# Kernel tuning notes

Hardware: AMD Instinct MI355X
Metric: run time of the kernel (lower is better)

Reference implementation:

```python
import jax, jax.numpy as jnp
import numpy as np

B, N, D, H = 2, 2048, 2048, 16
HD = D // H  # head_dim = 128


def _rope(x, cos, sin):
    # x: [B,H,N,HD]; cos/sin: [N,HD]. use_real=True, use_real_unbind_dim=-1 (interleaved pairs).
    xr = x[..., 0::2]
    xi = x[..., 1::2]
    x_rot = jnp.stack([-xi, xr], axis=-1).reshape(x.shape)
    return x * cos[None, None] + x_rot * sin[None, None]


def setup_inputs() -> dict:
    key = jax.random.key(0)
    ks = jax.random.split(key, 10)
    x = jax.random.normal(ks[0], (B, N, D), dtype=jnp.float32)
    # realistic RoPE tables
    inv_freq = 1.0 / (10000.0 ** (np.arange(0, HD, 2, dtype=np.float32) / HD))
    t = np.arange(N, dtype=np.float32)
    ang = np.einsum('n,f->nf', t, inv_freq)           # [N, HD/2]
    ang = np.repeat(ang, 2, axis=-1)                  # [N, HD] interleaved
    cos = jnp.asarray(np.cos(ang))
    sin = jnp.asarray(np.sin(ang))
    s = 0.02
    Wq = jax.random.normal(ks[1], (D, D), dtype=jnp.float32) * s
    Wk = jax.random.normal(ks[2], (D, D), dtype=jnp.float32) * s
    Wv = jax.random.normal(ks[3], (D, D), dtype=jnp.float32) * s
    Wo = jax.random.normal(ks[4], (D, D), dtype=jnp.float32) * s
    bq = jnp.zeros((D,), jnp.float32)
    bk = jnp.zeros((D,), jnp.float32)
    bv = jnp.zeros((D,), jnp.float32)
    bo = jnp.zeros((D,), jnp.float32)
    return {"x": x, "cos": cos, "sin": sin, "Wq": Wq, "bq": bq, "Wk": Wk,
            "bk": bk, "Wv": Wv, "bv": bv, "Wo": Wo, "bo": bo}


def reference(x, cos, sin, Wq, bq, Wk, bk, Wv, bv, Wo, bo):
    scale = HD ** -0.5
    q = x @ Wq + bq
    k = x @ Wk + bk
    v = x @ Wv + bv
    # b n (h c) -> b h n c
    def split_heads(t):
        return t.reshape(B, N, H, HD).transpose(0, 2, 1, 3)
    q, k, v = split_heads(q), split_heads(k), split_heads(v)
    q = q * scale  # module's dp_scale
    q = _rope(q, cos, sin)
    k = _rope(k, cos, sin)
    # flash_attn_func(softmax_scale=None) applies head_dim^-0.5 AGAIN -> effective HD^-1
    logits = jnp.einsum('bhqc,bhkc->bhqk', q, k) * scale
    attn = jax.nn.softmax(logits, axis=-1)
    o = jnp.einsum('bhqk,bhkc->bhqc', attn, v)
    o = o.transpose(0, 2, 1, 3).reshape(B, N, D)  # b h n c -> b n (h c)
    return o @ Wo + bo
```

## Files before the change

kernel.cpp:

```cpp
#include <hip/hip_runtime.h>

typedef unsigned short u16;
typedef __attribute__((ext_vector_type(8))) short bfx8;
typedef __attribute__((ext_vector_type(4))) float fx4;
typedef __attribute__((ext_vector_type(4))) unsigned short u16x4;

#define MFMA_BF16(a,b,c) __builtin_amdgcn_mfma_f32_16x16x32_bf16((a),(b),(c),0,0,0)

#define BATCH 2
#define SEQ   2048
#define DM    2048
#define NH    16
#define HD    128
#define MR    4096

__device__ __forceinline__ u16 f2bf(float f){
  union{float f; unsigned u;} v; v.f = f;
  unsigned r = v.u + 0x7FFFu + ((v.u >> 16) & 1u);
  return (u16)(r >> 16);
}
__device__ __forceinline__ unsigned cvtpk(float lo, float hi){
  unsigned r;
  asm("v_cvt_pk_bf16_f32 %0, %1, %2" : "=v"(r) : "v"(lo), "v"(hi));
  return r;
}
__device__ __forceinline__ void gll16(const void* g, void* l){
  __builtin_amdgcn_global_load_lds(
      (const __attribute__((address_space(1))) void*)g,
      (__attribute__((address_space(3))) void*)l, 16, 0, 0);
}

__global__ __launch_bounds__(256) void k_cast(const float* __restrict__ in,
                                              u16* __restrict__ o, int n4){
  int gid = blockIdx.x*256 + threadIdx.x;
  if (gid >= n4) return;
  float4 x = ((const float4*)in)[gid];
  u16x4 v = {f2bf(x.x), f2bf(x.y), f2bf(x.z), f2bf(x.w)};
  ((u16x4*)o)[gid] = v;
}

__global__ __launch_bounds__(256) void k_twcat(const float* __restrict__ Wq,
                                               const float* __restrict__ Wk,
                                               const float* __restrict__ Wv,
                                               u16* __restrict__ Th){
  __shared__ float T[64][65];
  int z = blockIdx.z;
  const float* W = (z==0) ? Wq : (z==1) ? Wk : Wv;
  int n0 = blockIdx.x*64, k0 = blockIdx.y*64;
  int t = threadIdx.x;
  int r = t>>2, c = (t&3)*16;
  const float* src = W + (size_t)(k0+r)*DM + n0 + c;
  #pragma unroll
  for (int j=0;j<4;j++){
    float4 v = *(const float4*)(src + 4*j);
    T[r][c+4*j+0]=v.x; T[r][c+4*j+1]=v.y; T[r][c+4*j+2]=v.z; T[r][c+4*j+3]=v.w;
  }
  __syncthreads();
  int nr = t>>2, kc = (t&3)*16;
  size_t ob = (size_t)(z*DM + n0+nr)*DM + k0 + kc;
  #pragma unroll
  for (int j=0;j<16;j+=4){
    u16x4 vh;
    #pragma unroll
    for (int q=0;q<4;q++) vh[q] = f2bf(T[kc+j+q][nr]);
    *(u16x4*)(Th+ob+j)=vh;
  }
}

__global__ __launch_bounds__(256) void k_tw(const float* __restrict__ W, u16* __restrict__ Th){
  __shared__ float T[64][65];
  int n0 = blockIdx.x*64, k0 = blockIdx.y*64;
  int t = threadIdx.x;
  int r = t>>2, c = (t&3)*16;
  const float* src = W + (size_t)(k0+r)*DM + n0 + c;
  #pragma unroll
  for (int j=0;j<4;j++){
    float4 v = *(const float4*)(src + 4*j);
    T[r][c+4*j+0]=v.x; T[r][c+4*j+1]=v.y; T[r][c+4*j+2]=v.z; T[r][c+4*j+3]=v.w;
  }
  __syncthreads();
  int nr = t>>2, kc = (t&3)*16;
  size_t ob = (size_t)(n0+nr)*DM + k0 + kc;
  #pragma unroll
  for (int j=0;j<16;j+=4){
    u16x4 vh;
    #pragma unroll
    for (int q=0;q<4;q++) vh[q] = f2bf(T[kc+j+q][nr]);
    *(u16x4*)(Th+ob+j)=vh;
  }
}

__global__ __launch_bounds__(256) void k_gemm_qkv(
    const u16* __restrict__ A, const u16* __restrict__ B,
    const float* __restrict__ bqp, const float* __restrict__ bkp, const float* __restrict__ bvp,
    const float* __restrict__ cs, const float* __restrict__ sn,
    u16* __restrict__ qb, u16* __restrict__ kb, u16* __restrict__ vt)
{
  __shared__ u16 sA[128*64], sB[128*64];
  const int K = DM;
  const int tid = threadIdx.x;
  const int lane = tid & 63;
  const int w = tid >> 6;
  const int g = lane >> 4, qi = lane & 15;
  const int wr = w >> 1, wc = w & 1;
  const int bm = blockIdx.y * 128;
  const int bn = blockIdx.x * 128;

  int r_[4], sc_[4];
  #pragma unroll
  for (int i=0;i<4;i++){
    int off = w*4096 + i*1024 + lane*16;
    int r = off>>7, cb = off&127;
    r_[i] = r; sc_[i] = (cb ^ ((r&7)<<4)) >> 1;
  }

  fx4 acc[4][4] = {};

  for (int k0 = 0; k0 < K; k0 += 64){
    __syncthreads();
    #pragma unroll
    for (int i=0;i<4;i++){
      gll16(A + (size_t)(bm + r_[i])*K + k0 + sc_[i], &sA[w*2048 + i*512]);
      gll16(B + (size_t)(bn + r_[i])*K + k0 + sc_[i], &sB[w*2048 + i*512]);
    }
    __syncthreads();

    #pragma unroll
    for (int kk=0;kk<2;kk++){
      const int cb = kk*64 + g*16;
      bfx8 fa[4], fb[4];
      #pragma unroll
      for (int m=0;m<4;m++){
        int row = wr*64 + m*16 + qi;
        fa[m] = *(const bfx8*)((const char*)sA + row*128 + (cb ^ ((row&7)<<4)));
      }
      #pragma unroll
      for (int n=0;n<4;n++){
        int row = wc*64 + n*16 + qi;
        fb[n] = *(const bfx8*)((const char*)sB + row*128 + (cb ^ ((row&7)<<4)));
      }
      #pragma unroll
      for (int m=0;m<4;m++)
        #pragma unroll
        for (int n=0;n<4;n++)
          acc[m][n] = MFMA_BF16(fa[m], fb[n], acc[m][n]);
    }
  }

  const int sec = bn >> 11;
  if (sec < 2){
    u16* dst = sec ? kb : qb;
    const float* bias = sec ? bkp : bqp;
    const float qs = sec ? 1.0f : (1.4426950408889634f/128.0f);
    #pragma unroll
    for (int m=0;m<4;m++){
      #pragma unroll
      for (int n=0;n<4;n++){
        int col = bn + wc*64 + n*16 + qi;
        int cq = col & 2047, hh = cq>>7, d = cq&127;
        float bc = bias[cq];
        float sgn = (d&1) ? 1.0f : -1.0f;
        #pragma unroll
        for (int r=0;r<4;r++){
          int row = bm + wr*64 + m*16 + g*4 + r;
          int bI = row>>11, nr2 = row&2047;
          float v = (acc[m][n][r] + bc)*qs;
          float p = __shfl_xor(v, 1, 64);
          float c = cs[nr2*HD + d], s = sn[nr2*HD + d];
          float y = v*c + sgn*p*s;
          dst[((size_t)(bI*NH+hh)*SEQ + nr2)*HD + d] = f2bf(y);
        }
      }
    }
  } else {
    #pragma unroll
    for (int m=0;m<4;m++){
      #pragma unroll
      for (int n=0;n<4;n++){
        int col = bn + wc*64 + n*16 + qi;
        int cv = col & 2047, hh = cv>>7, d = cv&127;
        float bc = bvp[cv];
        int row0 = bm + wr*64 + m*16 + g*4;
        int bI = row0>>11, n0_ = row0&2047;
        u16x4 pk;
        #pragma unroll
        for (int r=0;r<4;r++) pk[r] = f2bf(acc[m][n][r] + bc);
        *(u16x4*)(vt + ((size_t)(bI*NH+hh)*HD + d)*SEQ + n0_) = pk;
      }
    }
  }
}

__global__ __launch_bounds__(256) void k_gemm(
    const u16* __restrict__ A, const u16* __restrict__ B,
    const float* __restrict__ bias, float* __restrict__ C,
    int M, int N, int K)
{
  __shared__ u16 sA[128*64], sB[128*64];
  const int tid = threadIdx.x;
  const int lane = tid & 63;
  const int w = tid >> 6;
  const int g = lane >> 4, qi = lane & 15;
  const int wr = w >> 1, wc = w & 1;
  const int bm = blockIdx.y * 128;
  const int bn = blockIdx.x * 128;

  int r_[4], sc_[4];
  #pragma unroll
  for (int i=0;i<4;i++){
    int off = w*4096 + i*1024 + lane*16;
    int r = off>>7, cb = off&127;
    r_[i] = r; sc_[i] = (cb ^ ((r&7)<<4)) >> 1;
  }

  fx4 acc[4][4] = {};

  for (int k0 = 0; k0 < K; k0 += 64){
    __syncthreads();
    #pragma unroll
    for (int i=0;i<4;i++){
      gll16(A + (size_t)(bm + r_[i])*K + k0 + sc_[i], &sA[w*2048 + i*512]);
      gll16(B + (size_t)(bn + r_[i])*K + k0 + sc_[i], &sB[w*2048 + i*512]);
    }
    __syncthreads();

    #pragma unroll
    for (int kk=0;kk<2;kk++){
      const int cb = kk*64 + g*16;
      bfx8 fa[4], fb[4];
      #pragma unroll
      for (int m=0;m<4;m++){
        int row = wr*64 + m*16 + qi;
        fa[m] = *(const bfx8*)((const char*)sA + row*128 + (cb ^ ((row&7)<<4)));
      }
      #pragma unroll
      for (int n=0;n<4;n++){
        int row = wc*64 + n*16 + qi;
        fb[n] = *(const bfx8*)((const char*)sB + row*128 + (cb ^ ((row&7)<<4)));
      }
      #pragma unroll
      for (int m=0;m<4;m++)
        #pragma unroll
        for (int n=0;n<4;n++)
          acc[m][n] = MFMA_BF16(fa[m], fb[n], acc[m][n]);
    }
  }

  #pragma unroll
  for (int m=0;m<4;m++){
    #pragma unroll
    for (int n=0;n<4;n++){
      int col = bn + wc*64 + n*16 + qi;
      float bc = bias[col];
      #pragma unroll
      for (int r=0;r<4;r++){
        int row = bm + wr*64 + m*16 + g*4 + r;
        C[(size_t)row*N + col] = acc[m][n][r] + bc;
      }
    }
  }
}

__global__ __launch_bounds__(256) void k_flash(const u16* __restrict__ Q, const u16* __restrict__ Kb,
                                               const u16* __restrict__ Vt, u16* __restrict__ O){
  __shared__ union SM {
    struct { u16 k[2][64*128]; u16 v[2][128*64]; } s;
    u16 ob[128*128];
  } sm;
  const int tid = threadIdx.x, lane = tid & 63, w = tid >> 6;
  const int bid = blockIdx.x;
  const int qt = bid & 15, h = (bid>>4)&15, b = bid>>8;
  const int bh = b*NH + h;
  const int qb0 = qt*128;
  const int g = lane >> 4, qi = lane & 15;

  bfx8 qf[2][4];
  #pragma unroll
  for (int j=0;j<2;j++){
    const u16* qp = Q + ((size_t)bh*SEQ + qb0 + w*32 + j*16 + qi)*HD + g*8;
    #pragma unroll
    for (int ks=0; ks<4; ++ks) qf[j][ks] = *(const bfx8*)(qp + ks*32);
  }

  size_t kbase[4], vbase[4];
  #pragma unroll
  for (int i=0;i<4;i++){
    int off = w*4096 + i*1024 + lane*16;
    int kr = off>>8, kc = off&255;
    int kcs = kc ^ ((kr&7)<<4);
    kbase[i] = ((size_t)bh*SEQ + kr)*HD + (kcs>>1);
    int vr = off>>7, vc = off&127;
    int vcs = vc ^ ((vr&7)<<4);
    vbase[i] = ((size_t)bh*HD + vr)*SEQ + (vcs>>1);
  }

#define STG(bf_, kv_, i_) \
    gll16(Kb + kbase[i_] + (size_t)(kv_)*HD, &sm.s.k[bf_][w*2048 + i_*512]); \
    gll16(Vt + vbase[i_] + (kv_),            &sm.s.v[bf_][w*2048 + i_*512]);
#define STAGE(bf_, kv_) do { STG(bf_,kv_,0) STG(bf_,kv_,1) STG(bf_,kv_,2) STG(bf_,kv_,3) } while(0)

  fx4 accO[2][8] = {};
  float mrun[2] = {-1e30f,-1e30f}, lrun[2] = {0.f,0.f};

  STAGE(0, 0);
  int buf = 0;

  for (int t=0; t<32; ++t){
    if (t < 31){
      STAGE(buf^1, (t+1)*64);
      asm volatile("s_waitcnt vmcnt(8)" ::: "memory");
    } else {
      asm volatile("s_waitcnt vmcnt(0)" ::: "memory");
    }
    __builtin_amdgcn_s_barrier();
    const u16* sk = sm.s.k[buf];
    const u16* sv = sm.s.v[buf];

    fx4 st[2][4] = {};
    __builtin_amdgcn_s_setprio(1);
    #pragma unroll
    for (int ks=0; ks<4; ++ks){
      bfx8 kf[4];
      #pragma unroll
      for (int n=0;n<4;n++){
        int row = n*16 + qi;
        int cb = ks*64 + g*16;
        kf[n] = *(const bfx8*)((const char*)sk + row*256 + (cb ^ ((row&7)<<4)));
      }
      #pragma unroll
      for (int n=0;n<4;n++){
        st[0][n] = MFMA_BF16(kf[n], qf[0][ks], st[0][n]);
        st[1][n] = MFMA_BF16(kf[n], qf[1][ks], st[1][n]);
      }
    }
    __builtin_amdgcn_s_setprio(0);

    float pmv[2];
    #pragma unroll
    for (int j=0;j<2;j++){
      float pm = st[j][0][0];
      #pragma unroll
      for (int n=0;n<4;n++)
        #pragma unroll
        for (int r=0;r<4;r++) pm = fmaxf(pm, st[j][n][r]);
      pm = fmaxf(pm, __shfl_xor(pm, 16, 64));
      pm = fmaxf(pm, __shfl_xor(pm, 32, 64));
      pmv[j] = pm;
    }
    if (!__all((pmv[0] <= mrun[0] + 11.0f) && (pmv[1] <= mrun[1] + 11.0f))){
      #pragma unroll
      for (int j=0;j<2;j++){
        float mn = fmaxf(mrun[j], pmv[j]);
        float al = exp2f(mrun[j] - mn);
        lrun[j] *= al;
        #pragma unroll
        for (int nn=0;nn<8;nn++) accO[j][nn] = accO[j][nn]*al;
        mrun[j] = mn;
      }
    }
    #pragma unroll
    for (int j=0;j<2;j++){
      float ps = 0.f;
      #pragma unroll
      for (int n=0;n<4;n++)
        #pragma unroll
        for (int r=0;r<4;r++){
          float p = exp2f(st[j][n][r] - mrun[j]);
          st[j][n][r] = p;
          ps += p;
        }
      ps += __shfl_xor(ps, 16, 64);
      ps += __shfl_xor(ps, 32, 64);
      lrun[j] += ps;
    }

    int pkl[2][4], pkh[2][4];
    #pragma unroll
    for (int j=0;j<2;j++)
      #pragma unroll
      for (int n=0;n<4;n++){
        pkl[j][n] = (int)cvtpk(st[j][n][0], st[j][n][1]);
        pkh[j][n] = (int)cvtpk(st[j][n][2], st[j][n][3]);
      }

    const int s0 = qi + 16*((2*g)&3);
    const int s1 = qi + 16*((2*g+1)&3);
    const bool hi = (g>>1) != 0;

    #pragma unroll
    for (int ks=0; ks<2; ++ks){
      bfx8 pv[2];
      #pragma unroll
      for (int j=0;j<2;j++){
        int cl0 = pkl[j][2*ks],   ch0 = pkh[j][2*ks];
        int cl1 = pkl[j][2*ks+1], ch1 = pkh[j][2*ks+1];
        int t00 = __shfl(cl0, s0, 64), t10 = __shfl(cl1, s0, 64);
        int t01 = __shfl(ch0, s0, 64), t11 = __shfl(ch1, s0, 64);
        int t02 = __shfl(cl0, s1, 64), t12 = __shfl(cl1, s1, 64);
        int t03 = __shfl(ch0, s1, 64), t13 = __shfl(ch1, s1, 64);
        union { bfx8 v; int u[4]; } pu;
        pu.u[0] = hi ? t10 : t00;
        pu.u[1] = hi ? t11 : t01;
        pu.u[2] = hi ? t12 : t02;
        pu.u[3] = hi ? t13 : t03;
        pv[j] = pu.v;
      }
      __builtin_amdgcn_s_setprio(1);
      #pragma unroll
      for (int nn=0;nn<8;nn++){
        int row = nn*16 + qi;
        int cb = ks*64 + g*16;
        bfx8 vf = *(const bfx8*)((const char*)sv + row*128 + (cb ^ ((row&7)<<4)));
        accO[0][nn] = MFMA_BF16(vf, pv[0], accO[0][nn]);
        accO[1][nn] = MFMA_BF16(vf, pv[1], accO[1][nn]);
      }
      __builtin_amdgcn_s_setprio(0);
    }
    __builtin_amdgcn_s_barrier();
    buf ^= 1;
  }
#undef STAGE
#undef STG

  #pragma unroll
  for (int j=0;j<2;j++){
    float inv = 1.0f / lrun[j];
    int q = w*32 + j*16 + qi;
    #pragma unroll
    for (int nn=0;nn<8;nn++)
      #pragma unroll
      for (int r=0;r<4;r++){
        int d = nn*16 + g*4 + r;
        *(u16*)((char*)sm.ob + q*256 + ((d*2) ^ ((q&7)<<4))) = f2bf(accO[j][nn][r]*inv);
      }
  }
  __syncthreads();
  {
    int q2 = tid>>1, c0 = (tid&1)*64;
    u16* dst = O + (size_t)(b*SEQ + qb0 + q2)*DM + h*HD + c0;
    #pragma unroll
    for (int jj=0;jj<8;jj++){
      int d0 = c0 + jj*8;
      bfx8 v = *(const bfx8*)((const char*)sm.ob + q2*256 + ((d0*2) ^ ((q2&7)<<4)));
      *(bfx8*)(dst + jj*8) = v;
    }
  }
}

extern "C" void kernel_launch(void* const* d_in, const int* in_sizes, int n_in,
                              void* d_out, int out_size, void* d_ws, size_t ws_size,
                              hipStream_t stream){
  (void)in_sizes; (void)n_in; (void)out_size; (void)ws_size;
  const float* x  = (const float*)d_in[0];
  const float* cs = (const float*)d_in[1];
  const float* sn = (const float*)d_in[2];
  const float* Wq = (const float*)d_in[3];
  const float* bq = (const float*)d_in[4];
  const float* Wk = (const float*)d_in[5];
  const float* bk = (const float*)d_in[6];
  const float* Wv = (const float*)d_in[7];
  const float* bv = (const float*)d_in[8];
  const float* Wo = (const float*)d_in[9];
  const float* bo = (const float*)d_in[10];
  float* out = (float*)d_out;

  char* ws = (char*)d_ws;
  const size_t MB = 1048576;
  u16* xb   = (u16*)(ws);
  u16* wt   = (u16*)(ws + 16*MB);
  u16* qb   = (u16*)(ws + 40*MB);
  u16* kb   = (u16*)(ws + 56*MB);
  u16* vt   = (u16*)(ws + 72*MB);
  u16* ob16 = (u16*)(ws + 88*MB);

  k_cast<<<8192,256,0,stream>>>(x, xb, 2097152);
  k_twcat<<<dim3(32,32,3),256,0,stream>>>(Wq, Wk, Wv, wt);
  k_gemm_qkv<<<dim3(48,32),256,0,stream>>>(xb, wt, bq, bk, bv, cs, sn, qb, kb, vt);

  k_flash<<<512,256,0,stream>>>(qb, kb, vt, ob16);

  k_tw<<<dim3(32,32),256,0,stream>>>(Wo, wt);
  k_gemm<<<dim3(16,32),256,0,stream>>>(ob16, wt, bo, out, MR, DM, DM);
}
```

Before: 355.8 us.

## Halve flash-attention tile to 64 query rows with single-buffered split K/V staging

The attention kernel now uses 2 waves and 64 query rows per block, with twice as many blocks. The double-buffered K/V shared memory becomes a single buffer. K for the next step is loaded right after the QK product, and V right after the PV product, with waits and barriers placed between the phases. Cross-lane max and sum shuffles are moved off the common path: the max is reduced only when a rescale is needed, and the row sum only once at the end. The smaller shared-memory footprint aims to raise occupancy, but it doubles how often K/V are loaded per query and shortens the window for hiding load latency.

```diff
diff --git a/kernel.cpp b/kernel.cpp
--- a/kernel.cpp
+++ b/kernel.cpp
@@ -261,17 +261,17 @@
   }
 }
 
-__global__ __launch_bounds__(256) void k_flash(const u16* __restrict__ Q, const u16* __restrict__ Kb,
+__global__ __launch_bounds__(128) void k_flash(const u16* __restrict__ Q, const u16* __restrict__ Kb,
                                                const u16* __restrict__ Vt, u16* __restrict__ O){
   __shared__ union SM {
-    struct { u16 k[2][64*128]; u16 v[2][128*64]; } s;
-    u16 ob[128*128];
+    struct { u16 k[64*128]; u16 v[128*64]; } s;
+    u16 ob[64*128];
   } sm;
   const int tid = threadIdx.x, lane = tid & 63, w = tid >> 6;
   const int bid = blockIdx.x;
-  const int qt = bid & 15, h = (bid>>4)&15, b = bid>>8;
+  const int qt = bid & 31, h = (bid>>5)&15, b = bid>>9;
   const int bh = b*NH + h;
-  const int qb0 = qt*128;
+  const int qb0 = qt*64;
   const int g = lane >> 4, qi = lane & 15;
 
   bfx8 qf[2][4];
@@ -282,10 +282,10 @@
     for (int ks=0; ks<4; ++ks) qf[j][ks] = *(const bfx8*)(qp + ks*32);
   }
 
-  size_t kbase[4], vbase[4];
-  #pragma unroll
-  for (int i=0;i<4;i++){
-    int off = w*4096 + i*1024 + lane*16;
+  size_t kbase[8], vbase[8];
+  #pragma unroll
+  for (int i=0;i<8;i++){
+    int off = w*8192 + i*1024 + lane*16;
     int kr = off>>8, kc = off&255;
     int kcs = kc ^ ((kr&7)<<4);
     kbase[i] = ((size_t)bh*SEQ + kr)*HD + (kcs>>1);
@@ -294,27 +294,21 @@
     vbase[i] = ((size_t)bh*HD + vr)*SEQ + (vcs>>1);
   }
 
-#define STG(bf_, kv_, i_) \
-    gll16(Kb + kbase[i_] + (size_t)(kv_)*HD, &sm.s.k[bf_][w*2048 + i_*512]); \
-    gll16(Vt + vbase[i_] + (kv_),            &sm.s.v[bf_][w*2048 + i_*512]);
-#define STAGE(bf_, kv_) do { STG(bf_,kv_,0) STG(bf_,kv_,1) STG(bf_,kv_,2) STG(bf_,kv_,3) } while(0)
+#define STAGE_K(kv_) do { _Pragma("unroll") \
+    for (int i_=0;i_<8;i_++) gll16(Kb + kbase[i_] + (size_t)(kv_)*HD, &sm.s.k[w*4096 + i_*512]); } while(0)
+#define STAGE_V(kv_) do { _Pragma("unroll") \
+    for (int i_=0;i_<8;i_++) gll16(Vt + vbase[i_] + (kv_),            &sm.s.v[w*4096 + i_*512]); } while(0)
 
   fx4 accO[2][8] = {};
-  float mrun[2] = {-1e30f,-1e30f}, lrun[2] = {0.f,0.f};
-
-  STAGE(0, 0);
-  int buf = 0;
+  float mrun[2] = {-1e30f,-1e30f};
+  float lrun[2] = {0.f,0.f};
+
+  STAGE_K(0);
+  STAGE_V(0);
 
   for (int t=0; t<32; ++t){
-    if (t < 31){
-      STAGE(buf^1, (t+1)*64);
-      asm volatile("s_waitcnt vmcnt(8)" ::: "memory");
-    } else {
-      asm volatile("s_waitcnt vmcnt(0)" ::: "memory");
-    }
+    asm volatile("s_waitcnt vmcnt(8)" ::: "memory");
     __builtin_amdgcn_s_barrier();
-    const u16* sk = sm.s.k[buf];
-    const u16* sv = sm.s.v[buf];
 
     fx4 st[2][4] = {};
     __builtin_amdgcn_s_setprio(1);
@@ -325,7 +319,7 @@
       for (int n=0;n<4;n++){
         int row = n*16 + qi;
         int cb = ks*64 + g*16;
-        kf[n] = *(const bfx8*)((const char*)sk + row*256 + (cb ^ ((row&7)<<4)));
+        kf[n] = *(const bfx8*)((const char*)sm.s.k + row*256 + (cb ^ ((row&7)<<4)));
       }
       #pragma unroll
       for (int n=0;n<4;n++){
@@ -334,6 +328,8 @@
       }
     }
     __builtin_amdgcn_s_setprio(0);
+    __builtin_amdgcn_s_barrier();
+    if (t < 31) STAGE_K(t*64 + 64);
 
     float pmv[2];
     #pragma unroll
@@ -343,14 +339,15 @@
       for (int n=0;n<4;n++)
         #pragma unroll
         for (int r=0;r<4;r++) pm = fmaxf(pm, st[j][n][r]);
-      pm = fmaxf(pm, __shfl_xor(pm, 16, 64));
-      pm = fmaxf(pm, __shfl_xor(pm, 32, 64));
       pmv[j] = pm;
     }
     if (!__all((pmv[0] <= mrun[0] + 11.0f) && (pmv[1] <= mrun[1] + 11.0f))){
       #pragma unroll
       for (int j=0;j<2;j++){
-        float mn = fmaxf(mrun[j], pmv[j]);
+        float pq = pmv[j];
+        pq = fmaxf(pq, __shfl_xor(pq, 16, 64));
+        pq = fmaxf(pq, __shfl_xor(pq, 32, 64));
+        float mn = fmaxf(mrun[j], pq);
         float al = exp2f(mrun[j] - mn);
         lrun[j] *= al;
         #pragma unroll
@@ -369,8 +366,6 @@
           st[j][n][r] = p;
           ps += p;
         }
-      ps += __shfl_xor(ps, 16, 64);
-      ps += __shfl_xor(ps, 32, 64);
       lrun[j] += ps;
     }
 
@@ -382,6 +377,10 @@
         pkl[j][n] = (int)cvtpk(st[j][n][0], st[j][n][1]);
         pkh[j][n] = (int)cvtpk(st[j][n][2], st[j][n][3]);
       }
+
+    if (t < 31) asm volatile("s_waitcnt vmcnt(8)" ::: "memory");
+    else        asm volatile("s_waitcnt vmcnt(0)" ::: "memory");
+    __builtin_amdgcn_s_barrier();
 
     const int s0 = qi + 16*((2*g)&3);
     const int s1 = qi + 16*((2*g+1)&3);
@@ -410,21 +409,24 @@
       for (int nn=0;nn<8;nn++){
         int row = nn*16 + qi;
         int cb = ks*64 + g*16;
-        bfx8 vf = *(const bfx8*)((const char*)sv + row*128 + (cb ^ ((row&7)<<4)));
+        bfx8 vf = *(const bfx8*)((const char*)sm.s.v + row*128 + (cb ^ ((row&7)<<4)));
         accO[0][nn] = MFMA_BF16(vf, pv[0], accO[0][nn]);
         accO[1][nn] = MFMA_BF16(vf, pv[1], accO[1][nn]);
       }
       __builtin_amdgcn_s_setprio(0);
     }
     __builtin_amdgcn_s_barrier();
-    buf ^= 1;
-  }
-#undef STAGE
-#undef STG
+    if (t < 31) STAGE_V(t*64 + 64);
+  }
+#undef STAGE_K
+#undef STAGE_V
 
   #pragma unroll
   for (int j=0;j<2;j++){
-    float inv = 1.0f / lrun[j];
+    float l = lrun[j];
+    l += __shfl_xor(l, 16, 64);
+    l += __shfl_xor(l, 32, 64);
+    float inv = 1.0f / l;
     int q = w*32 + j*16 + qi;
     #pragma unroll
     for (int nn=0;nn<8;nn++)
@@ -477,7 +479,7 @@
   k_twcat<<<dim3(32,32,3),256,0,stream>>>(Wq, Wk, Wv, wt);
   k_gemm_qkv<<<dim3(48,32),256,0,stream>>>(xb, wt, bq, bk, bv, cs, sn, qb, kb, vt);
 
-  k_flash<<<512,256,0,stream>>>(qb, kb, vt, ob16);
+  k_flash<<<1024,128,0,stream>>>(qb, kb, vt, ob16);
 
   k_tw<<<dim3(32,32),256,0,stream>>>(Wo, wt);
   k_gemm<<<dim3(16,32),256,0,stream>>>(ob16, wt, bo, out, MR, DM, DM);
```

After: 343.4 us. -3.5%, faster.
